# Performance work log

Measured on AMD Instinct MI355X. Metric: run time of the kernel, lower is better.

The kernel has to match this reference:

```python
import jax, jax.numpy as jnp
import numpy as np

NUMOBJECTS, EMB, H, E, T = 1000, 128, 128, 8, 2
N = 4096

def _ln(x, g, b, eps=1e-5):
    mu = jnp.mean(x, axis=-1, keepdims=True)
    var = jnp.var(x, axis=-1, keepdims=True)
    return (x - mu) * jax.lax.rsqrt(var + eps) * g + b

def setup_inputs() -> dict:
    key = jax.random.key(0)
    ks = jax.random.split(key, 16)
    s = lambda fan_in: 1.0 / np.sqrt(fan_in)
    return {
        "adjacency_matrix": jax.random.uniform(ks[0], (E, N, N), jnp.float32),
        "node_states": jax.random.normal(ks[1], (N, 2 * EMB), jnp.float32),
        "node_ids": jax.random.randint(ks[2], (N,), 0, NUMOBJECTS),
        "emb_table": jax.random.normal(ks[3], (NUMOBJECTS, EMB), jnp.float32) * 0.02,
        "W_init": jax.random.normal(ks[4], (3 * EMB, H), jnp.float32) * s(3 * EMB),
        "b_init": jnp.zeros((H,), jnp.float32),
        "W_out": jax.random.normal(ks[5], (E, H, H), jnp.float32) * s(H),
        "b_out": jnp.zeros((E, H), jnp.float32),
        "W_in": jax.random.normal(ks[6], (E, H, H), jnp.float32) * s(H),
        "b_in": jnp.zeros((E, H), jnp.float32),
        "Wx": jax.random.normal(ks[7], (2 * E * H, 3 * H), jnp.float32) * s(2 * E * H),
        "bx": jnp.zeros((3 * H,), jnp.float32),
        "Wh": jax.random.normal(ks[8], (H, 3 * H), jnp.float32) * s(H),
        "bh": jnp.zeros((3 * H,), jnp.float32),
        "ln_gamma": jnp.ones((3, H), jnp.float32),
        "ln_beta": jnp.zeros((3, H), jnp.float32),
    }

def _gru(x, h, Wx, bx, Wh, bh, g, b):
    gi = x @ Wx + bx                      # [N, 3H]
    gh = h @ Wh + bh                      # [N, 3H]
    ir, iz, inn = jnp.split(gi, 3, axis=-1)
    hr, hz, hn = jnp.split(gh, 3, axis=-1)
    r = jax.nn.sigmoid(_ln(ir + hr, g[0], b[0]))
    z = jax.nn.sigmoid(_ln(iz + hz, g[1], b[1]))
    n = jnp.tanh(_ln(inn + r * hn, g[2], b[2]))
    return (1.0 - z) * n + z * h

def reference(adjacency_matrix, node_states, node_ids, emb_table, W_init, b_init,
              W_out, b_out, W_in, b_in, Wx, bx, Wh, bh, ln_gamma, ln_beta):
    emb = emb_table[node_ids]                                   # [N, EMB]
    node_init = jnp.concatenate([emb, node_states], axis=1)     # [N, 3*EMB]
    h = jnp.tanh(node_init @ W_init + b_init)                   # [N, H]
    A_out = adjacency_matrix                                    # [E, N, N]
    A_in = jnp.transpose(adjacency_matrix, (0, 2, 1))
    n_nodes = h.shape[0]
    for _ in range(T):
        # grouped per-edge-type FC + Tanh, then adjacency message passing
        ho = jnp.tanh(jnp.einsum('nh,ehk->enk', h, W_out) + b_out[:, None, :])
        mo = jnp.einsum('enm,emk->nek', A_out, ho).reshape(n_nodes, -1)  # [N, E*H]
        hi = jnp.tanh(jnp.einsum('nh,ehk->enk', h, W_in) + b_in[:, None, :])
        mi = jnp.einsum('enm,emk->nek', A_in, hi).reshape(n_nodes, -1)
        msg = jnp.concatenate([mo, mi], axis=1)                 # [N, 2*E*H]
        h = _gru(msg, h, Wx, bx, Wh, bh, ln_gamma, ln_beta)
    return h
```

## Files before the change

kernel.cpp:

```cpp
#include <hip/hip_runtime.h>
#include <stdint.h>

#define NNODES 4096
#define HDIM   128
#define NE     8
#define KXX    2176
#define NG     512
#define NKT    34

typedef unsigned short u16;
typedef _Float16 f16;
typedef f16   h8v __attribute__((ext_vector_type(8)));
typedef float f4v __attribute__((ext_vector_type(4)));

static __device__ __forceinline__ u16 hbits(f16 h) {
    union { f16 h; u16 u; } x; x.h = h; return x.u;
}
static __device__ __forceinline__ int swz(int r, int c) {
    return r * 64 + (c ^ ((((r >> 3) ^ r) & 7) << 3));
}
static __device__ __forceinline__ f4v mfma16h(h8v a, h8v b, f4v c) {
    return __builtin_amdgcn_mfma_f32_16x16x32_f16(a, b, c, 0, 0, 0);
}
static __device__ __forceinline__ h8v lds_frag(const u16* p) {
    return *(const h8v*)p;
}
static __device__ __forceinline__ void ncvt8h(const float* g, u16* vh) {
    float4 v0 = *(const float4*)g, v1 = *(const float4*)(g + 4);
    float vs[8] = {v0.x, v0.y, v0.z, v0.w, v1.x, v1.y, v1.z, v1.w};
    #pragma unroll
    for (int q = 0; q < 8; q++) vh[q] = hbits((f16)vs[q]);
}
static __device__ __forceinline__ void stage_tile(const u16* __restrict__ g, u16* l, int tid) {
    const int lane = tid & 63, wv = tid >> 6;
    #pragma unroll
    for (int q = 0; q < 4; q++) {
        __builtin_amdgcn_global_load_lds(
            (__attribute__((address_space(1))) void*)(g + ((size_t)((wv * 4 + q) * 64 + lane)) * 8),
            (__attribute__((address_space(3))) void*)(l + (wv * 4 + q) * 512),
            16, 0, 0);
    }
}

__global__ void k0_init(const float* __restrict__ nst, const int* __restrict__ ids,
                        const float* __restrict__ emb, const float* __restrict__ Wi,
                        const float* __restrict__ bi, float* __restrict__ h,
                        float* __restrict__ X)
{
    __shared__ float ni[16][384];
    const int n0 = blockIdx.x * 16;
    const int tid = threadIdx.x;
    for (int idx = tid; idx < 16 * 384; idx += 128) {
        int r = idx / 384, c = idx - r * 384;
        float v;
        if (c < 128) v = emb[(size_t)ids[n0 + r] * 128 + c];
        else         v = nst[(size_t)(n0 + r) * 256 + (c - 128)];
        ni[r][c] = v;
    }
    __syncthreads();
    float acc[16];
    #pragma unroll
    for (int r = 0; r < 16; r++) acc[r] = 0.f;
    for (int c = 0; c < 384; c++) {
        float w = Wi[c * 128 + tid];
        #pragma unroll
        for (int r = 0; r < 16; r++) acc[r] += ni[r][c] * w;
    }
    float bb = bi[tid];
    #pragma unroll
    for (int r = 0; r < 16; r++) {
        float v = tanhf(acc[r] + bb);
        h[(size_t)(n0 + r) * HDIM + tid] = v;
        X[(size_t)(n0 + r) * KXX + 2048 + tid] = v;
    }
}

__global__ void kprep(const float* __restrict__ Wx, const float* __restrict__ bx,
                      const float* __restrict__ Wh, const float* __restrict__ bh,
                      u16* __restrict__ WTt, float* __restrict__ bv)
{
    const int j = blockIdx.x;
    const int ct = j >> 7, jl = j & 127;
    for (int c = threadIdx.x; c < KXX; c += blockDim.x) {
        float v;
        if (j < 384) {
            if (c < 2048) v = Wx[(size_t)c * 384 + j];
            else          v = (j < 256) ? Wh[(size_t)(c - 2048) * 384 + j] : 0.f;
        } else {
            if (c < 2048) v = 0.f;
            else          v = Wh[(size_t)(c - 2048) * 384 + (j - 128)];
        }
        WTt[(size_t)(ct * NKT + (c >> 6)) * 8192 + swz(jl, c & 63)] = hbits((f16)v);
    }
    if (threadIdx.x == 0) {
        float b;
        if (j < 256)      b = bx[j] + bh[j];
        else if (j < 384) b = bx[j];
        else              b = bh[j - 128];
        bv[j] = b;
    }
}

__global__ void kprepW(const float* __restrict__ Wo, const float* __restrict__ Wn,
                       u16* __restrict__ Wp)
{
    const int de = blockIdx.x;
    const int dir = de >> 3, e = de & 7;
    const float* W = (dir ? Wn : Wo) + (size_t)e * HDIM * HDIM;
    u16* dst = Wp + (size_t)de * 2 * 8192;
    for (int idx = threadIdx.x; idx < HDIM * HDIM; idx += blockDim.x) {
        int j = idx >> 7, k = idx & 127;
        dst[(size_t)(j >> 6) * 8192 + swz(k, j & 63)] = hbits((f16)W[idx]);
    }
}

__global__ void kpa(const float* __restrict__ A, u16* __restrict__ AT0,
                    u16* __restrict__ AT1)
{
    const int b = blockIdx.x;
    const int mb = b & 63, nt = (b >> 6) & 31, e = b >> 11;
    __shared__ u16 lf[64 * 136];
    const int tid = threadIdx.x;
    {
        const int rr = tid >> 2, cb = (tid & 3) * 32;
        const float* src = A + (size_t)e * NNODES * NNODES
                             + (size_t)(mb * 64 + rr) * NNODES + nt * 128 + cb;
        u16 hv[32];
        #pragma unroll
        for (int q = 0; q < 8; q++) {
            float4 v = *(const float4*)(src + q * 4);
            hv[q * 4 + 0] = hbits((f16)v.x); hv[q * 4 + 1] = hbits((f16)v.y);
            hv[q * 4 + 2] = hbits((f16)v.z); hv[q * 4 + 3] = hbits((f16)v.w);
        }
        const int arow = mb * 64 + rr;
        const int mc0 = nt * 2 + (cb >> 6), cl0 = cb & 63;
        const size_t tb0 = (((size_t)e * 32 + (arow >> 7)) * 64 + mc0) * 8192;
        const int rl = arow & 127;
        #pragma unroll
        for (int g = 0; g < 4; g++)
            *(uint4*)&AT0[tb0 + swz(rl, cl0 + 8 * g)] = *(const uint4*)&hv[8 * g];
        #pragma unroll
        for (int g = 0; g < 4; g++)
            *(uint4*)&lf[rr * 136 + cb + 8 * g] = *(const uint4*)&hv[8 * g];
    }
    __syncthreads();
    {
        const size_t tb1 = (((size_t)e * 32 + nt) * 64 + mb) * 8192;
        const int r = tid >> 3, c = (tid & 7) * 8;
        #pragma unroll
        for (int p = 0; p < 4; p++) {
            const int nl = r + 32 * p;
            u16 vv[8];
            #pragma unroll
            for (int q = 0; q < 8; q++) vv[q] = lf[(c + q) * 136 + nl];
            *(uint4*)&AT1[tb1 + swz(nl, c)] = *(const uint4*)vv;
        }
    }
}

__global__ __launch_bounds__(256, 3) void k1_hoT(const float* __restrict__ h,
        const u16* __restrict__ Wp, const float* __restrict__ bo,
        const float* __restrict__ bn, u16* __restrict__ hoT)
{
    const int mt = blockIdx.x, e = blockIdx.y, dir = blockIdx.z;
    const float* bias = (dir == 0 ? bo : bn) + (size_t)e * HDIM;
    const u16* Wt = Wp + (size_t)(dir * NE + e) * 2 * 8192;
    const int m0 = mt * 128;
    const int tid = threadIdx.x, lane = tid & 63, wv = tid >> 6;
    const int wrow0 = (wv & 1) * 64, wcol0 = (wv >> 1) * 64;
    const int lrow = lane & 15, lkb = (lane >> 4) * 8;

    __shared__ __align__(16) u16 lWT[128 * 64];
    __shared__ __align__(16) u16 lB [128 * 64];

    f4v acc[4][4];
    #pragma unroll
    for (int i = 0; i < 4; i++)
        #pragma unroll
        for (int j = 0; j < 4; j++)
            #pragma unroll
            for (int q = 0; q < 4; q++) acc[i][j][q] = 0.f;

    for (int jt = 0; jt < 128; jt += 64) {
        __syncthreads();
        stage_tile(Wt + (size_t)(jt >> 6) * 8192, lWT, tid);
        {
            int m = tid >> 3;
            int jc = (tid & 7) * 8;
            #pragma unroll
            for (int p = 0; p < 4; p++) {
                u16 vh[8];
                ncvt8h(h + (size_t)(m0 + m + 32 * p) * HDIM + jt + jc, vh);
                *(uint4*)&lB[swz(m + 32 * p, jc)] = *(const uint4*)vh;
            }
        }
        __syncthreads();
        #pragma unroll
        for (int ks = 0; ks < 2; ks++) {
            const int kb = ks * 32 + lkb;
            h8v a[4], b8[4];
            #pragma unroll
            for (int i = 0; i < 4; i++)
                a[i] = lds_frag(&lWT[swz(wrow0 + 16 * i + lrow, kb)]);
            #pragma unroll
            for (int j = 0; j < 4; j++)
                b8[j] = lds_frag(&lB[swz(wcol0 + 16 * j + lrow, kb)]);
            #pragma unroll
            for (int i = 0; i < 4; i++)
                #pragma unroll
                for (int j = 0; j < 4; j++)
                    acc[i][j] = mfma16h(a[i], b8[j], acc[i][j]);
        }
    }
    u16* dst = hoT + (size_t)(dir * NE + e) * 64 * 8192;
    #pragma unroll
    for (int i = 0; i < 4; i++)
        #pragma unroll
        for (int j = 0; j < 4; j++)
            #pragma unroll
            for (int reg = 0; reg < 4; reg++) {
                int k = wrow0 + 16 * i + (lane >> 4) * 4 + reg;
                int m = m0 + wcol0 + 16 * j + (lane & 15);
                float v = tanhf(acc[i][j][reg] + bias[k]);
                dst[(size_t)(m >> 6) * 8192 + swz(k, m & 63)] = hbits((f16)v);
            }
}

__global__ __launch_bounds__(256, 4) void k2n(const float* __restrict__ A,
        const u16* __restrict__ AT0, const u16* __restrict__ AT1,
        const u16* __restrict__ hoT, float* __restrict__ X0,
        float* __restrict__ X1, float* __restrict__ X2, int nsplit, int pre)
{
    const int l = blockIdx.x;
    const int x = l & 7, i = l >> 3;
    const int c = x * 2 * nsplit + (i >> 5), nt = i & 31;
    const int e = c & 7, dir = (c >> 3) & 1, kk = c >> 4;
    const int n0 = nt * 128;
    int ms0, ms1;
    if (nsplit == 1) { ms0 = 0; ms1 = 64; }
    else { ms0 = (kk == 0) ? 0 : (kk == 1 ? 22 : 43);
           ms1 = (kk == 0) ? 22 : (kk == 1 ? 43 : 64); }
    const int tid = threadIdx.x, lane = tid & 63, wv = tid >> 6;
    const int wrow0 = (wv & 1) * 64, wcol0 = (wv >> 1) * 64;
    const int lrow = lane & 15, lkb = (lane >> 4) * 8;

    __shared__ __align__(16) u16 lA[128 * 64];
    __shared__ __align__(16) u16 lB[128 * 64];

    const float* Ae = A + (size_t)e * NNODES * NNODES;
    const u16* Bt0 = hoT + (size_t)(dir * NE + e) * 64 * 8192;
    const u16* Tp  = (dir ? AT1 : AT0) + (((size_t)e * 32 + nt) * 64) * 8192;

    f4v acc[4][4];
    #pragma unroll
    for (int ii = 0; ii < 4; ii++)
        #pragma unroll
        for (int j = 0; j < 4; j++)
            #pragma unroll
            for (int q = 0; q < 4; q++) acc[ii][j][q] = 0.f;

    for (int mc = ms0; mc < ms1; mc++) {
        const int m0 = mc * 64;
        __syncthreads();
        stage_tile(Bt0 + (size_t)mc * 8192, lB, tid);
        if (pre) {
            stage_tile(Tp + (size_t)mc * 8192, lA, tid);
        } else if (dir == 0) {
            const int r = tid >> 3, cc = (tid & 7) * 8;
            #pragma unroll
            for (int p = 0; p < 4; p++) {
                u16 vh[8];
                ncvt8h(Ae + (size_t)(n0 + r + 32 * p) * NNODES + m0 + cc, vh);
                *(uint4*)&lA[swz(r + 32 * p, cc)] = *(const uint4*)vh;
            }
        } else {
            const int mm = tid >> 4, nn = (tid & 15) * 8;
            #pragma unroll
            for (int p = 0; p < 4; p++) {
                u16 vh[8];
                ncvt8h(Ae + (size_t)(m0 + mm + 16 * p) * NNODES + n0 + nn, vh);
                #pragma unroll
                for (int q = 0; q < 8; q++)
                    lA[swz(nn + q, mm + 16 * p)] = vh[q];
            }
        }
        __syncthreads();
        #pragma unroll
        for (int ks = 0; ks < 2; ks++) {
            const int kb = ks * 32 + lkb;
            h8v ah[4], b8[4];
            #pragma unroll
            for (int ii = 0; ii < 4; ii++)
                ah[ii] = lds_frag(&lA[swz(wrow0 + 16 * ii + lrow, kb)]);
            #pragma unroll
            for (int j = 0; j < 4; j++)
                b8[j] = lds_frag(&lB[swz(wcol0 + 16 * j + lrow, kb)]);
            #pragma unroll
            for (int ii = 0; ii < 4; ii++)
                #pragma unroll
                for (int j = 0; j < 4; j++)
                    acc[ii][j] = mfma16h(ah[ii], b8[j], acc[ii][j]);
        }
    }
    float* Xp; size_t st;
    if (kk == 0)      { Xp = X0; st = KXX; }
    else if (kk == 1) { Xp = X1; st = 2048; }
    else              { Xp = X2; st = 2048; }
    const size_t cb = (size_t)(dir * 1024 + e * 128);
    #pragma unroll
    for (int ii = 0; ii < 4; ii++)
        #pragma unroll
        for (int j = 0; j < 4; j++)
            #pragma unroll
            for (int reg = 0; reg < 4; reg++) {
                int row = wrow0 + 16 * ii + (lane >> 4) * 4 + reg;
                int col = wcol0 + 16 * j + (lane & 15);
                Xp[(size_t)(n0 + row) * st + cb + col] = acc[ii][j][reg];
            }
}

__global__ __launch_bounds__(256, 4) void k3_gates(const float* __restrict__ X,
        const float* __restrict__ X1, const float* __restrict__ X2,
        const u16* __restrict__ WTt, const float* __restrict__ bv,
        float* __restrict__ G, int nsplit)
{
    const int nt = blockIdx.x, ct = blockIdx.y;
    const int n0 = nt * 64, j0 = ct * 128;
    const int tid = threadIdx.x, lane = tid & 63, wv = tid >> 6;
    const int wrow0 = (wv & 1) * 32, wcol0 = (wv >> 1) * 64;
    const int lrow = lane & 15, lkb = (lane >> 4) * 8;
    __shared__ __align__(16) u16 lX[64 * 64];
    __shared__ __align__(16) u16 lW[128 * 64];

    f4v acc[2][4];
    #pragma unroll
    for (int i = 0; i < 2; i++)
        #pragma unroll
        for (int j = 0; j < 4; j++)
            #pragma unroll
            for (int q = 0; q < 4; q++) acc[i][j][q] = 0.f;

    for (int kt = 0; kt < NKT; kt++) {
        const int c0 = kt * 64;
        __syncthreads();
        stage_tile(WTt + (size_t)(ct * NKT + kt) * 8192, lW, tid);
        {
            const int r = tid >> 3, cc = (tid & 7) * 8;
            #pragma unroll
            for (int p = 0; p < 2; p++) {
                const int row = r + 32 * p;
                float vs[8];
                {
                    const float* xs = X + (size_t)(n0 + row) * KXX + c0 + cc;
                    float4 a0 = *(const float4*)xs, a1 = *(const float4*)(xs + 4);
                    vs[0]=a0.x; vs[1]=a0.y; vs[2]=a0.z; vs[3]=a0.w;
                    vs[4]=a1.x; vs[5]=a1.y; vs[6]=a1.z; vs[7]=a1.w;
                }
                if (nsplit == 3 && c0 < 2048) {
                    const size_t o = (size_t)(n0 + row) * 2048 + c0 + cc;
                    float4 b0 = *(const float4*)(X1 + o), b1 = *(const float4*)(X1 + o + 4);
                    float4 d0 = *(const float4*)(X2 + o), d1 = *(const float4*)(X2 + o + 4);
                    vs[0]+=b0.x+d0.x; vs[1]+=b0.y+d0.y; vs[2]+=b0.z+d0.z; vs[3]+=b0.w+d0.w;
                    vs[4]+=b1.x+d1.x; vs[5]+=b1.y+d1.y; vs[6]+=b1.z+d1.z; vs[7]+=b1.w+d1.w;
                }
                u16 vh[8];
                #pragma unroll
                for (int q = 0; q < 8; q++) vh[q] = hbits((f16)vs[q]);
                *(uint4*)&lX[swz(row, cc)] = *(const uint4*)vh;
            }
        }
        __syncthreads();
        #pragma unroll
        for (int ks = 0; ks < 2; ks++) {
            const int kb = ks * 32 + lkb;
            h8v ah[2], b8[4];
            #pragma unroll
            for (int i = 0; i < 2; i++)
                ah[i] = lds_frag(&lX[swz(wrow0 + 16 * i + lrow, kb)]);
            #pragma unroll
            for (int j = 0; j < 4; j++)
                b8[j] = lds_frag(&lW[swz(wcol0 + 16 * j + lrow, kb)]);
            #pragma unroll
            for (int i = 0; i < 2; i++)
                #pragma unroll
                for (int j = 0; j < 4; j++)
                    acc[i][j] = mfma16h(ah[i], b8[j], acc[i][j]);
        }
    }
    #pragma unroll
    for (int i = 0; i < 2; i++)
        #pragma unroll
        for (int j = 0; j < 4; j++)
            #pragma unroll
            for (int reg = 0; reg < 4; reg++) {
                int row = wrow0 + 16 * i + (lane >> 4) * 4 + reg;
                int col = wcol0 + 16 * j + (lane & 15);
                G[(size_t)(n0 + row) * NG + j0 + col] = acc[i][j][reg] + bv[j0 + col];
            }
}

__global__ void k4_ln(const float* __restrict__ G, const float* __restrict__ gam,
                      const float* __restrict__ bet, float* __restrict__ h,
                      float* __restrict__ X, float* __restrict__ out)
{
    const int n = blockIdx.x * 4 + (threadIdx.x >> 6);
    const int t = threadIdx.x & 63;
    const float* g = G + (size_t)n * NG;
    float a0 = g[t],       a0b = g[t + 64];
    float a1 = g[128 + t], a1b = g[192 + t];
    float a2 = g[256 + t], a2b = g[320 + t];
    float a3 = g[384 + t], a3b = g[448 + t];

    auto redsum = [](float v) {
        #pragma unroll
        for (int m = 32; m >= 1; m >>= 1) v += __shfl_xor(v, m, 64);
        return v;
    };

    float s0 = redsum(a0 + a0b) * (1.f / 128.f);
    float q0 = redsum(a0 * a0 + a0b * a0b) * (1.f / 128.f);
    float rs0 = rsqrtf(fmaxf(q0 - s0 * s0, 0.f) + 1e-5f);
    float x0  = (a0  - s0) * rs0 * gam[t]      + bet[t];
    float x0b = (a0b - s0) * rs0 * gam[t + 64] + bet[t + 64];
    float r  = 1.f / (1.f + expf(-x0));
    float rb = 1.f / (1.f + expf(-x0b));

    float s1 = redsum(a1 + a1b) * (1.f / 128.f);
    float q1 = redsum(a1 * a1 + a1b * a1b) * (1.f / 128.f);
    float rs1 = rsqrtf(fmaxf(q1 - s1 * s1, 0.f) + 1e-5f);
    float x1  = (a1  - s1) * rs1 * gam[128 + t] + bet[128 + t];
    float x1b = (a1b - s1) * rs1 * gam[192 + t] + bet[192 + t];
    float z  = 1.f / (1.f + expf(-x1));
    float zb = 1.f / (1.f + expf(-x1b));

    float c2  = a2  + r  * a3;
    float c2b = a2b + rb * a3b;
    float s2 = redsum(c2 + c2b) * (1.f / 128.f);
    float q2 = redsum(c2 * c2 + c2b * c2b) * (1.f / 128.f);
    float rs2 = rsqrtf(fmaxf(q2 - s2 * s2, 0.f) + 1e-5f);
    float x2  = (c2  - s2) * rs2 * gam[256 + t] + bet[256 + t];
    float x2b = (c2b - s2) * rs2 * gam[320 + t] + bet[320 + t];
    float nn  = tanhf(x2);
    float nnb = tanhf(x2b);

    float ho  = h[(size_t)n * HDIM + t];
    float hob = h[(size_t)n * HDIM + t + 64];
    float hn  = (1.f - z)  * nn  + z  * ho;
    float hnb = (1.f - zb) * nnb + zb * hob;
    h[(size_t)n * HDIM + t]      = hn;
    h[(size_t)n * HDIM + t + 64] = hnb;
    X[(size_t)n * KXX + 2048 + t]      = hn;
    X[(size_t)n * KXX + 2048 + t + 64] = hnb;
    out[(size_t)n * HDIM + t]      = hn;
    out[(size_t)n * HDIM + t + 64] = hnb;
}

extern "C" void kernel_launch(void* const* d_in, const int* in_sizes, int n_in,
                              void* d_out, int out_size, void* d_ws, size_t ws_size,
                              hipStream_t stream)
{
    const float* A    = (const float*)d_in[0];
    const float* nst  = (const float*)d_in[1];
    const int*   ids  = (const int*)d_in[2];
    const float* emb  = (const float*)d_in[3];
    const float* Wi   = (const float*)d_in[4];
    const float* bi   = (const float*)d_in[5];
    const float* Wo   = (const float*)d_in[6];
    const float* bo   = (const float*)d_in[7];
    const float* Wn   = (const float*)d_in[8];
    const float* bn   = (const float*)d_in[9];
    const float* Wx   = (const float*)d_in[10];
    const float* bx   = (const float*)d_in[11];
    const float* Wh   = (const float*)d_in[12];
    const float* bh   = (const float*)d_in[13];
    const float* gam  = (const float*)d_in[14];
    const float* bet  = (const float*)d_in[15];

    char* ws = (char*)d_ws;
    size_t off = 0;
    auto alloc = [&](size_t bytes) {
        size_t cur = off; off += (bytes + 255) & ~(size_t)255; return (void*)(ws + cur);
    };
    float* h   = (float*)alloc((size_t)NNODES * HDIM * 4);
    u16*   hoT = (u16*)  alloc((size_t)2 * NE * 64 * 8192 * 2);
    float* X   = (float*)alloc((size_t)NNODES * KXX * 4);
    float* G   = (float*)alloc((size_t)NNODES * NG * 4);
    u16*   WTt = (u16*)  alloc((size_t)4 * NKT * 8192 * 2);
    float* bv  = (float*)alloc((size_t)NG * 4);
    u16*   Wp  = (u16*)  alloc((size_t)16 * 2 * 8192 * 2);
    size_t need0 = off;
    float* X1  = (float*)alloc((size_t)NNODES * 2048 * 4);
    float* X2  = (float*)alloc((size_t)NNODES * 2048 * 4);
    size_t need1 = off;
    u16*   AT0 = (u16*)  alloc((size_t)NE * NNODES * NNODES * 2);
    u16*   AT1 = (u16*)  alloc((size_t)NE * NNODES * NNODES * 2);
    size_t need2 = off;

    int nsplit, pre;
    if      (ws_size >= need2) { nsplit = 3; pre = 1; }
    else if (ws_size >= need1) { nsplit = 3; pre = 0; }
    else if (ws_size >= need0) { nsplit = 1; pre = 0; }
    else return;

    kprep<<<512, 256, 0, stream>>>(Wx, bx, Wh, bh, WTt, bv);
    kprepW<<<16, 256, 0, stream>>>(Wo, Wn, Wp);
    k0_init<<<256, 128, 0, stream>>>(nst, ids, emb, Wi, bi, h, X);
    if (pre) kpa<<<16384, 256, 0, stream>>>(A, AT0, AT1);
    for (int it = 0; it < 2; it++) {
        k1_hoT<<<dim3(32, 8, 2), 256, 0, stream>>>(h, Wp, bo, bn, hoT);
        k2n<<<512 * nsplit, 256, 0, stream>>>(A, AT0, AT1, hoT, X, X1, X2, nsplit, pre);
        k3_gates<<<dim3(64, 4), 256, 0, stream>>>(X, X1, X2, WTt, bv, G, nsplit);
        k4_ln<<<1024, 256, 0, stream>>>(G, gam, bet, h, X, (float*)d_out);
    }
    (void)in_sizes; (void)n_in; (void)out_size;
}
```

Measured before the change: 1.414 ms.

## Store messages as pre-swizzled fp16 tiles and split gate GEMM over K

The message-passing kernel now uses 64-row output tiles over the full m range instead of a 3-way K split with fp32 partial buffers. It writes results directly as fp16 in the swizzled tile layout that the gate GEMM loads via global_load_lds. This removes the fp32 X/X1/X2 traffic and the per-tile conversion in k3. The gate GEMM is split in two along K into G0/G1, which doubles its grid, and the bias is folded into the LN kernel. The costs are less reuse of hoT per A tile in k2n and an extra G buffer to read.

Measured after the change: 1.294 ms. 1.09x faster.

```diff
diff --git a/kernel.cpp b/kernel.cpp
--- a/kernel.cpp
+++ b/kernel.cpp
@@ -16,6 +16,9 @@
 static __device__ __forceinline__ u16 hbits(f16 h) {
     union { f16 h; u16 u; } x; x.h = h; return x.u;
 }
+static __device__ __forceinline__ f16 h_of(u16 u) {
+    union { u16 u; f16 h; } x; x.u = u; return x.h;
+}
 static __device__ __forceinline__ int swz(int r, int c) {
     return r * 64 + (c ^ ((((r >> 3) ^ r) & 7) << 3));
 }
@@ -31,7 +34,7 @@
     #pragma unroll
     for (int q = 0; q < 8; q++) vh[q] = hbits((f16)vs[q]);
 }
-static __device__ __forceinline__ void stage_tile(const u16* __restrict__ g, u16* l, int tid) {
+static __device__ __forceinline__ void stage_tile16(const u16* __restrict__ g, u16* l, int tid) {
     const int lane = tid & 63, wv = tid >> 6;
     #pragma unroll
     for (int q = 0; q < 4; q++) {
@@ -41,11 +44,21 @@
             16, 0, 0);
     }
 }
+static __device__ __forceinline__ void stage_tile8(const u16* __restrict__ g, u16* l, int tid) {
+    const int lane = tid & 63, wv = tid >> 6;
+    #pragma unroll
+    for (int q = 0; q < 2; q++) {
+        __builtin_amdgcn_global_load_lds(
+            (__attribute__((address_space(1))) void*)(g + ((size_t)((wv * 2 + q) * 64 + lane)) * 8),
+            (__attribute__((address_space(3))) void*)(l + (wv * 2 + q) * 512),
+            16, 0, 0);
+    }
+}
 
 __global__ void k0_init(const float* __restrict__ nst, const int* __restrict__ ids,
                         const float* __restrict__ emb, const float* __restrict__ Wi,
                         const float* __restrict__ bi, float* __restrict__ h,
-                        float* __restrict__ X)
+                        u16* __restrict__ Xh)
 {
     __shared__ float ni[16][384];
     const int n0 = blockIdx.x * 16;
@@ -67,11 +80,13 @@
         for (int r = 0; r < 16; r++) acc[r] += ni[r][c] * w;
     }
     float bb = bi[tid];
+    const int kt = 32 + (tid >> 6), cl = tid & 63;
     #pragma unroll
     for (int r = 0; r < 16; r++) {
+        const int n = n0 + r;
         float v = tanhf(acc[r] + bb);
-        h[(size_t)(n0 + r) * HDIM + tid] = v;
-        X[(size_t)(n0 + r) * KXX + 2048 + tid] = v;
+        h[(size_t)n * HDIM + tid] = v;
+        Xh[(size_t)(n >> 6) * NKT * 4096 + kt * 4096 + swz(n & 63, cl)] = hbits((f16)v);
     }
 }
 
@@ -183,7 +198,7 @@
 
     for (int jt = 0; jt < 128; jt += 64) {
         __syncthreads();
-        stage_tile(Wt + (size_t)(jt >> 6) * 8192, lWT, tid);
+        stage_tile16(Wt + (size_t)(jt >> 6) * 8192, lWT, tid);
         {
             int m = tid >> 3;
             int jc = (tid & 7) * 8;
@@ -228,104 +243,98 @@
 
 __global__ __launch_bounds__(256, 4) void k2n(const float* __restrict__ A,
         const u16* __restrict__ AT0, const u16* __restrict__ AT1,
-        const u16* __restrict__ hoT, float* __restrict__ X0,
-        float* __restrict__ X1, float* __restrict__ X2, int nsplit, int pre)
+        const u16* __restrict__ hoT, u16* __restrict__ Xh, int pre)
 {
     const int l = blockIdx.x;
     const int x = l & 7, i = l >> 3;
-    const int c = x * 2 * nsplit + (i >> 5), nt = i & 31;
-    const int e = c & 7, dir = (c >> 3) & 1, kk = c >> 4;
-    const int n0 = nt * 128;
-    int ms0, ms1;
-    if (nsplit == 1) { ms0 = 0; ms1 = 64; }
-    else { ms0 = (kk == 0) ? 0 : (kk == 1 ? 22 : 43);
-           ms1 = (kk == 0) ? 22 : (kk == 1 ? 43 : 64); }
+    const int c = x * 2 + (i >> 6), nt64 = i & 63;
+    const int e = c & 7, dir = c >> 3;
+    const int n0 = nt64 * 64;
     const int tid = threadIdx.x, lane = tid & 63, wv = tid >> 6;
-    const int wrow0 = (wv & 1) * 64, wcol0 = (wv >> 1) * 64;
+    const int wrow0 = (wv & 1) * 32, wcol0 = (wv >> 1) * 64;
     const int lrow = lane & 15, lkb = (lane >> 4) * 8;
 
-    __shared__ __align__(16) u16 lA[128 * 64];
+    __shared__ __align__(16) u16 lA[64 * 64];
     __shared__ __align__(16) u16 lB[128 * 64];
 
     const float* Ae = A + (size_t)e * NNODES * NNODES;
     const u16* Bt0 = hoT + (size_t)(dir * NE + e) * 64 * 8192;
-    const u16* Tp  = (dir ? AT1 : AT0) + (((size_t)e * 32 + nt) * 64) * 8192;
-
-    f4v acc[4][4];
-    #pragma unroll
-    for (int ii = 0; ii < 4; ii++)
+    const u16* Tp  = (dir ? AT1 : AT0)
+                   + (((size_t)e * 32 + (nt64 >> 1)) * 64) * 8192 + (nt64 & 1) * 4096;
+
+    f4v acc[2][4];
+    #pragma unroll
+    for (int ii = 0; ii < 2; ii++)
         #pragma unroll
         for (int j = 0; j < 4; j++)
             #pragma unroll
             for (int q = 0; q < 4; q++) acc[ii][j][q] = 0.f;
 
-    for (int mc = ms0; mc < ms1; mc++) {
+    for (int mc = 0; mc < 64; mc++) {
         const int m0 = mc * 64;
         __syncthreads();
-        stage_tile(Bt0 + (size_t)mc * 8192, lB, tid);
+        stage_tile16(Bt0 + (size_t)mc * 8192, lB, tid);
         if (pre) {
-            stage_tile(Tp + (size_t)mc * 8192, lA, tid);
+            stage_tile8(Tp + (size_t)mc * 8192, lA, tid);
         } else if (dir == 0) {
-            const int r = tid >> 3, cc = (tid & 7) * 8;
-            #pragma unroll
-            for (int p = 0; p < 4; p++) {
+            const int r = tid >> 2, cc = (tid & 3) * 16;
+            #pragma unroll
+            for (int p = 0; p < 2; p++) {
                 u16 vh[8];
-                ncvt8h(Ae + (size_t)(n0 + r + 32 * p) * NNODES + m0 + cc, vh);
-                *(uint4*)&lA[swz(r + 32 * p, cc)] = *(const uint4*)vh;
+                ncvt8h(Ae + (size_t)(n0 + r) * NNODES + m0 + cc + 8 * p, vh);
+                *(uint4*)&lA[swz(r, cc + 8 * p)] = *(const uint4*)vh;
             }
         } else {
-            const int mm = tid >> 4, nn = (tid & 15) * 8;
-            #pragma unroll
-            for (int p = 0; p < 4; p++) {
+            const int mm = tid >> 2, nn = (tid & 3) * 16;
+            #pragma unroll
+            for (int p = 0; p < 2; p++) {
                 u16 vh[8];
-                ncvt8h(Ae + (size_t)(m0 + mm + 16 * p) * NNODES + n0 + nn, vh);
+                ncvt8h(Ae + (size_t)(m0 + mm) * NNODES + n0 + nn + 8 * p, vh);
                 #pragma unroll
                 for (int q = 0; q < 8; q++)
-                    lA[swz(nn + q, mm + 16 * p)] = vh[q];
+                    lA[swz(nn + 8 * p + q, mm)] = vh[q];
             }
         }
         __syncthreads();
         #pragma unroll
         for (int ks = 0; ks < 2; ks++) {
             const int kb = ks * 32 + lkb;
-            h8v ah[4], b8[4];
-            #pragma unroll
-            for (int ii = 0; ii < 4; ii++)
+            h8v ah[2], b8[4];
+            #pragma unroll
+            for (int ii = 0; ii < 2; ii++)
                 ah[ii] = lds_frag(&lA[swz(wrow0 + 16 * ii + lrow, kb)]);
             #pragma unroll
             for (int j = 0; j < 4; j++)
                 b8[j] = lds_frag(&lB[swz(wcol0 + 16 * j + lrow, kb)]);
             #pragma unroll
-            for (int ii = 0; ii < 4; ii++)
+            for (int ii = 0; ii < 2; ii++)
                 #pragma unroll
                 for (int j = 0; j < 4; j++)
                     acc[ii][j] = mfma16h(ah[ii], b8[j], acc[ii][j]);
         }
     }
-    float* Xp; size_t st;
-    if (kk == 0)      { Xp = X0; st = KXX; }
-    else if (kk == 1) { Xp = X1; st = 2048; }
-    else              { Xp = X2; st = 2048; }
-    const size_t cb = (size_t)(dir * 1024 + e * 128);
-    #pragma unroll
-    for (int ii = 0; ii < 4; ii++)
+    u16* xt = Xh + (size_t)nt64 * NKT * 4096;
+    #pragma unroll
+    for (int ii = 0; ii < 2; ii++)
         #pragma unroll
         for (int j = 0; j < 4; j++)
             #pragma unroll
             for (int reg = 0; reg < 4; reg++) {
                 int row = wrow0 + 16 * ii + (lane >> 4) * 4 + reg;
-                int col = wcol0 + 16 * j + (lane & 15);
-                Xp[(size_t)(n0 + row) * st + cb + col] = acc[ii][j][reg];
+                int C = dir * 1024 + e * 128 + wcol0 + 16 * j + (lane & 15);
+                xt[(size_t)(C >> 6) * 4096 + swz(row, C & 63)] =
+                    hbits((f16)acc[ii][j][reg]);
             }
 }
 
-__global__ __launch_bounds__(256, 4) void k3_gates(const float* __restrict__ X,
-        const float* __restrict__ X1, const float* __restrict__ X2,
-        const u16* __restrict__ WTt, const float* __restrict__ bv,
-        float* __restrict__ G, int nsplit)
-{
-    const int nt = blockIdx.x, ct = blockIdx.y;
+__global__ __launch_bounds__(256, 4) void k3_gates(const u16* __restrict__ Xh,
+        const u16* __restrict__ WTt, float* __restrict__ G0,
+        float* __restrict__ G1)
+{
+    const int nt = blockIdx.x, ct = blockIdx.y, kk = blockIdx.z;
     const int n0 = nt * 64, j0 = ct * 128;
+    const int kt0 = kk ? 17 : 0, kt1 = kk ? NKT : 17;
+    float* G = kk ? G1 : G0;
     const int tid = threadIdx.x, lane = tid & 63, wv = tid >> 6;
     const int wrow0 = (wv & 1) * 32, wcol0 = (wv >> 1) * 64;
     const int lrow = lane & 15, lkb = (lane >> 4) * 8;
@@ -340,35 +349,10 @@
             #pragma unroll
             for (int q = 0; q < 4; q++) acc[i][j][q] = 0.f;
 
-    for (int kt = 0; kt < NKT; kt++) {
-        const int c0 = kt * 64;
+    for (int kt = kt0; kt < kt1; kt++) {
         __syncthreads();
-        stage_tile(WTt + (size_t)(ct * NKT + kt) * 8192, lW, tid);
-        {
-            const int r = tid >> 3, cc = (tid & 7) * 8;
-            #pragma unroll
-            for (int p = 0; p < 2; p++) {
-                const int row = r + 32 * p;
-                float vs[8];
-                {
-                    const float* xs = X + (size_t)(n0 + row) * KXX + c0 + cc;
-                    float4 a0 = *(const float4*)xs, a1 = *(const float4*)(xs + 4);
-                    vs[0]=a0.x; vs[1]=a0.y; vs[2]=a0.z; vs[3]=a0.w;
-                    vs[4]=a1.x; vs[5]=a1.y; vs[6]=a1.z; vs[7]=a1.w;
-                }
-                if (nsplit == 3 && c0 < 2048) {
-                    const size_t o = (size_t)(n0 + row) * 2048 + c0 + cc;
-                    float4 b0 = *(const float4*)(X1 + o), b1 = *(const float4*)(X1 + o + 4);
-                    float4 d0 = *(const float4*)(X2 + o), d1 = *(const float4*)(X2 + o + 4);
-                    vs[0]+=b0.x+d0.x; vs[1]+=b0.y+d0.y; vs[2]+=b0.z+d0.z; vs[3]+=b0.w+d0.w;
-                    vs[4]+=b1.x+d1.x; vs[5]+=b1.y+d1.y; vs[6]+=b1.z+d1.z; vs[7]+=b1.w+d1.w;
-                }
-                u16 vh[8];
-                #pragma unroll
-                for (int q = 0; q < 8; q++) vh[q] = hbits((f16)vs[q]);
-                *(uint4*)&lX[swz(row, cc)] = *(const uint4*)vh;
-            }
-        }
+        stage_tile8(Xh + ((size_t)nt * NKT + kt) * 4096, lX, tid);
+        stage_tile16(WTt + (size_t)(ct * NKT + kt) * 8192, lW, tid);
         __syncthreads();
         #pragma unroll
         for (int ks = 0; ks < 2; ks++) {
@@ -395,21 +379,24 @@
             for (int reg = 0; reg < 4; reg++) {
                 int row = wrow0 + 16 * i + (lane >> 4) * 4 + reg;
                 int col = wcol0 + 16 * j + (lane & 15);
-                G[(size_t)(n0 + row) * NG + j0 + col] = acc[i][j][reg] + bv[j0 + col];
+                G[(size_t)(n0 + row) * NG + j0 + col] = acc[i][j][reg];
             }
 }
 
-__global__ void k4_ln(const float* __restrict__ G, const float* __restrict__ gam,
+__global__ void k4_ln(const float* __restrict__ G0, const float* __restrict__ G1,
+                      const float* __restrict__ bv, const float* __restrict__ gam,
                       const float* __restrict__ bet, float* __restrict__ h,
-                      float* __restrict__ X, float* __restrict__ out)
+                      u16* __restrict__ Xh, float* __restrict__ out)
 {
     const int n = blockIdx.x * 4 + (threadIdx.x >> 6);
     const int t = threadIdx.x & 63;
-    const float* g = G + (size_t)n * NG;
-    float a0 = g[t],       a0b = g[t + 64];
-    float a1 = g[128 + t], a1b = g[192 + t];
-    float a2 = g[256 + t], a2b = g[320 + t];
-    float a3 = g[384 + t], a3b = g[448 + t];
+    const float* g0 = G0 + (size_t)n * NG;
+    const float* g1 = G1 + (size_t)n * NG;
+    auto gv = [&](int c) { return g0[c] + g1[c] + bv[c]; };
+    float a0 = gv(t),       a0b = gv(t + 64);
+    float a1 = gv(128 + t), a1b = gv(192 + t);
+    float a2 = gv(256 + t), a2b = gv(320 + t);
+    float a3 = gv(384 + t), a3b = gv(448 + t);
 
     auto redsum = [](float v) {
         #pragma unroll
@@ -449,8 +436,9 @@
     float hnb = (1.f - zb) * nnb + zb * hob;
     h[(size_t)n * HDIM + t]      = hn;
     h[(size_t)n * HDIM + t + 64] = hnb;
-    X[(size_t)n * KXX + 2048 + t]      = hn;
-    X[(size_t)n * KXX + 2048 + t + 64] = hnb;
+    u16* xt = Xh + (size_t)(n >> 6) * NKT * 4096;
+    xt[32 * 4096 + swz(n & 63, t)] = hbits((f16)hn);
+    xt[33 * 4096 + swz(n & 63, t)] = hbits((f16)hnb);
     out[(size_t)n * HDIM + t]      = hn;
     out[(size_t)n * HDIM + t + 64] = hnb;
 }
@@ -483,34 +471,31 @@
     };
     float* h   = (float*)alloc((size_t)NNODES * HDIM * 4);
     u16*   hoT = (u16*)  alloc((size_t)2 * NE * 64 * 8192 * 2);
-    float* X   = (float*)alloc((size_t)NNODES * KXX * 4);
-    float* G   = (float*)alloc((size_t)NNODES * NG * 4);
+    u16*   Xh  = (u16*)  alloc((size_t)64 * NKT * 4096 * 2);
+    float* G0  = (float*)alloc((size_t)NNODES * NG * 4);
+    float* G1  = (float*)alloc((size_t)NNODES * NG * 4);
     u16*   WTt = (u16*)  alloc((size_t)4 * NKT * 8192 * 2);
     float* bv  = (float*)alloc((size_t)NG * 4);
     u16*   Wp  = (u16*)  alloc((size_t)16 * 2 * 8192 * 2);
     size_t need0 = off;
-    float* X1  = (float*)alloc((size_t)NNODES * 2048 * 4);
-    float* X2  = (float*)alloc((size_t)NNODES * 2048 * 4);
-    size_t need1 = off;
     u16*   AT0 = (u16*)  alloc((size_t)NE * NNODES * NNODES * 2);
     u16*   AT1 = (u16*)  alloc((size_t)NE * NNODES * NNODES * 2);
-    size_t need2 = off;
-
-    int nsplit, pre;
-    if      (ws_size >= need2) { nsplit = 3; pre = 1; }
-    else if (ws_size >= need1) { nsplit = 3; pre = 0; }
-    else if (ws_size >= need0) { nsplit = 1; pre = 0; }
+    size_t need1 = off;
+
+    int pre;
+    if      (ws_size >= need1) pre = 1;
+    else if (ws_size >= need0) pre = 0;
     else return;
 
     kprep<<<512, 256, 0, stream>>>(Wx, bx, Wh, bh, WTt, bv);
     kprepW<<<16, 256, 0, stream>>>(Wo, Wn, Wp);
-    k0_init<<<256, 128, 0, stream>>>(nst, ids, emb, Wi, bi, h, X);
+    k0_init<<<256, 128, 0, stream>>>(nst, ids, emb, Wi, bi, h, Xh);
     if (pre) kpa<<<16384, 256, 0, stream>>>(A, AT0, AT1);
     for (int it = 0; it < 2; it++) {
         k1_hoT<<<dim3(32, 8, 2), 256, 0, stream>>>(h, Wp, bo, bn, hoT);
-        k2n<<<512 * nsplit, 256, 0, stream>>>(A, AT0, AT1, hoT, X, X1, X2, nsplit, pre);
-        k3_gates<<<dim3(64, 4), 256, 0, stream>>>(X, X1, X2, WTt, bv, G, nsplit);
-        k4_ln<<<1024, 256, 0, stream>>>(G, gam, bet, h, X, (float*)d_out);
+        k2n<<<1024, 256, 0, stream>>>(A, AT0, AT1, hoT, Xh, pre);
+        k3_gates<<<dim3(64, 4, 2), 256, 0, stream>>>(Xh, WTt, G0, G1);
+        k4_ln<<<1024, 256, 0, stream>>>(G0, G1, bv, gam, bet, h, Xh, (float*)d_out);
     }
     (void)in_sizes; (void)n_in; (void)out_size;
 }
```
